# Performance work log

Hardware: AMD Instinct MI355X
Metric: run time of the kernel (lower is better)

## Reference

```python
import jax, jax.numpy as jnp
import numpy as np

B, N, C = 64, 196, 768
H = 12
HD = C // H            # 64
TOPK = int(0.25 * HD)  # 16
HIDDEN = int(C * 4.0)  # 3072
SCALE = HD ** -0.5
EPS = 1e-5


def layernorm(x, g, b):
    mu = jnp.mean(x, axis=-1, keepdims=True)
    var = jnp.var(x, axis=-1, keepdims=True)
    return (x - mu) * jax.lax.rsqrt(var + EPS) * g + b


def setup_inputs() -> dict:
    key = jax.random.key(0)
    ks = jax.random.split(key, 8)
    s = 0.02
    return {
        "x": jax.random.normal(ks[0], (B, N, C), jnp.float32),
        "norm1_g": jnp.ones((C,), jnp.float32),
        "norm1_b": jnp.zeros((C,), jnp.float32),
        "qk_w": jax.random.normal(ks[1], (2 * C, C), jnp.float32) * s,   # torch Linear [out,in], no bias
        "attn_proj_w": jax.random.normal(ks[2], (C, H * TOPK), jnp.float32) * s,
        "attn_proj_b": jnp.zeros((C,), jnp.float32),
        "norm2_g": jnp.ones((C,), jnp.float32),
        "norm2_b": jnp.zeros((C,), jnp.float32),
        "fc1_w": jax.random.normal(ks[3], (HIDDEN, C), jnp.float32) * s,
        "fc1_b": jnp.zeros((HIDDEN,), jnp.float32),
        "fc2_w": jax.random.normal(ks[4], (C, HIDDEN), jnp.float32) * s,
        "fc2_b": jnp.zeros((C,), jnp.float32),
    }


def reference(x, norm1_g, norm1_b, qk_w, attn_proj_w, attn_proj_b,
              norm2_g, norm2_b, fc1_w, fc1_b, fc2_w, fc2_b):
    # --- HomoAttention branch ---
    h = layernorm(x, norm1_g, norm1_b)                       # [B,N,C]
    qk = h @ qk_w.T                                          # [B,N,2C]
    qk = qk.reshape(B, N, 2, H, HD).transpose(2, 0, 3, 1, 4) # [2,B,H,N,HD]
    q, k = qk[0] * SCALE, qk[1]
    attn = jnp.einsum('bhnd,bhmd->bhnm', q, k)               # [B,H,N,N]
    top_vals, _ = jax.lax.top_k(attn, TOPK)                  # [B,H,N,TOPK]
    a = jax.nn.softmax(top_vals, axis=-1)
    a = a.transpose(0, 2, 1, 3).reshape(B, N, H * TOPK)      # [B,N,H*TOPK]
    x = x + a @ attn_proj_w.T + attn_proj_b

    # --- MLP branch ---
    h2 = layernorm(x, norm2_g, norm2_b)
    h2 = jax.nn.gelu(h2 @ fc1_w.T + fc1_b, approximate=False)
    x = x + h2 @ fc2_w.T + fc2_b
    return x
```

## Files before the change

kernel.cpp:

```cpp
#include <hip/hip_runtime.h>


#define BATCH 64
#define SEQ   196
#define CH    768
#define NHEAD 12
#define HDIM  64
#define TOPK  16
#define HID   3072
#define MROWS 12544
#define MHALF 6272
#define SCALE_F 0.125f
#define NEGBIG -3e38f

typedef __bf16 bf16x8 __attribute__((ext_vector_type(8)));
typedef float  f32x4  __attribute__((ext_vector_type(4)));

__device__ __forceinline__ unsigned short f2b(float f) {
    union { float f; unsigned int i; } c; c.f = f;
    unsigned int u = c.i;
    return (unsigned short)((u + 0x7fffu + ((u >> 16) & 1u)) >> 16);
}
__device__ __forceinline__ float b2f(unsigned short u) {
    union { unsigned int i; float f; } c; c.i = ((unsigned int)u) << 16; return c.f;
}

__device__ __forceinline__ float med3(float a, float b, float c) {
    float r;
    asm("v_med3_f32 %0, %1, %2, %3" : "=v"(r) : "v"(a), "v"(b), "v"(c));
    return r;
}

__device__ __forceinline__ float gelu_f(float v) {
    float u = v * (0.7978845608f + 0.0356774081f * v * v);
    float e = __expf(2.0f * u);
    float th = 1.0f - 2.0f / (e + 1.0f);
    return 0.5f * v * (1.0f + th);
}

__device__ __forceinline__ void async16(const unsigned short* g, unsigned short* l) {
    __builtin_amdgcn_global_load_lds(
        (const __attribute__((address_space(1))) unsigned int*)(g),
        (__attribute__((address_space(3))) unsigned int*)(l), 16, 0, 0);
}

__global__ __launch_bounds__(256) void prep_k(const float* __restrict__ x,
                                              const float* __restrict__ gw,
                                              const float* __restrict__ bw,
                                              unsigned short* __restrict__ hbuf,
                                              const float* __restrict__ s0, unsigned short* __restrict__ d0, int n0,
                                              const float* __restrict__ s1, unsigned short* __restrict__ d1, int n1,
                                              const float* __restrict__ s2, unsigned short* __restrict__ d2, int n2,
                                              const float* __restrict__ s3, unsigned short* __restrict__ d3, int n3)
{
    const int bid = blockIdx.x;
    const int tid = threadIdx.x;
    __shared__ __align__(16) float red[8];
    if (bid < MROWS) {
        const float* xr = x + (size_t)bid * CH;
        float v0 = xr[tid], v1 = xr[tid + 256], v2 = xr[tid + 512];
        float s  = v0 + v1 + v2;
        float sq = v0*v0 + v1*v1 + v2*v2;
#pragma unroll
        for (int off = 32; off > 0; off >>= 1) {
            s  += __shfl_down(s, off, 64);
            sq += __shfl_down(sq, off, 64);
        }
        if ((tid & 63) == 0) { red[(tid >> 6) * 2] = s; red[(tid >> 6) * 2 + 1] = sq; }
        __syncthreads();
        s  = red[0] + red[2] + red[4] + red[6];
        sq = red[1] + red[3] + red[5] + red[7];
        float mu  = s * (1.0f / CH);
        float var = sq * (1.0f / CH) - mu * mu;
        float rs  = rsqrtf(var + 1e-5f);
        unsigned short* orow = hbuf + (size_t)bid * CH;
        orow[tid]       = f2b((v0 - mu) * rs * gw[tid]       + bw[tid]);
        orow[tid + 256] = f2b((v1 - mu) * rs * gw[tid + 256] + bw[tid + 256]);
        orow[tid + 512] = f2b((v2 - mu) * rs * gw[tid + 512] + bw[tid + 512]);
    } else {
        int idx = ((bid - MROWS) * 256 + tid) * 4;
        const float* s; unsigned short* d; int n;
        if (idx < n0) { s = s0; d = d0; n = n0; }
        else {
            idx -= n0;
            if (idx < n1) { s = s1; d = d1; n = n1; }
            else {
                idx -= n1;
                if (idx < n2) { s = s2; d = d2; n = n2; }
                else { idx -= n2; s = s3; d = d3; n = n3; }
            }
        }
        if (idx < n) {
            float4 v = *(const float4*)(s + idx);
            ushort4 o;
            o.x = f2b(v.x); o.y = f2b(v.y); o.z = f2b(v.z); o.w = f2b(v.w);
            *(ushort4*)(d + idx) = o;
        }
    }
}

template<bool INF32>
__global__ __launch_bounds__(256) void ln_k(const void* __restrict__ xin,
                                            const float* __restrict__ gw,
                                            const float* __restrict__ bw,
                                            unsigned short* __restrict__ out)
{
    const int row = blockIdx.x;
    const int tid = threadIdx.x;
    float v0, v1, v2;
    if constexpr (INF32) {
        const float* xr = (const float*)xin + (size_t)row * CH;
        v0 = xr[tid]; v1 = xr[tid + 256]; v2 = xr[tid + 512];
    } else {
        const unsigned short* xr = (const unsigned short*)xin + (size_t)row * CH;
        v0 = b2f(xr[tid]); v1 = b2f(xr[tid + 256]); v2 = b2f(xr[tid + 512]);
    }
    float s  = v0 + v1 + v2;
    float sq = v0*v0 + v1*v1 + v2*v2;
#pragma unroll
    for (int off = 32; off > 0; off >>= 1) {
        s  += __shfl_down(s, off, 64);
        sq += __shfl_down(sq, off, 64);
    }
    __shared__ __align__(16) float red[8];
    if ((tid & 63) == 0) { red[(tid >> 6) * 2] = s; red[(tid >> 6) * 2 + 1] = sq; }
    __syncthreads();
// ... 33 lines not shown
    const int remM = gridM - sg * 8;
    int mloc, nloc;
    if (remM >= 8) { mloc = sg * 8 + (r & 7); nloc = r >> 3; }
    else           { mloc = sg * 8 + r % remM; nloc = r / remM; }
    const int tileM = mloc * TM;
    const int tileN = nloc * TN;

    const int wm = (w / WCOLS) * 64;
    const int wn = (w % WCOLS) * (JF * 16);
    const int q   = lane >> 4;
    const int l16 = lane & 15;
    const int csw = (q ^ (l16 & 3)) * 8;

    f32x4 acc[4][JF];
#pragma unroll
    for (int i = 0; i < 4; ++i)
#pragma unroll
        for (int j = 0; j < JF; ++j) acc[i][j] = (f32x4){0.f, 0.f, 0.f, 0.f};

    const int r0 = tid >> 2;
    const int g0 = ((tid & 3) ^ (r0 & 3)) * 8;

    const unsigned short* pB[TN / 64];
    const unsigned short* pA[TM / 64];
#pragma unroll
    for (int c = 0; c < TN / 64; ++c) pB[c] = Bw + (size_t)(tileN + r0 + c * 64) * K + g0;
#pragma unroll
    for (int c = 0; c < TM / 64; ++c) pA[c] = A + (size_t)(tileM + r0 + c * 64) * K + g0;

    auto stage = [&](int buf) {
#pragma unroll
        for (int c = 0; c < TN / 64; ++c) {
            async16(pB[c], &Bs[buf][(size_t)(c * 256 + w * 64) * 8]);
            pB[c] += 32;
        }
#pragma unroll
        for (int c = 0; c < TM / 64; ++c) {
            async16(pA[c], &As[buf][(size_t)(c * 256 + w * 64) * 8]);
            pA[c] += 32;
        }
    };

    const int kIters = K >> 5;
    stage(0);
    int cur = 0;
    for (int kt = 0; kt < kIters; ++kt) {
        __syncthreads();
        if (kt + 1 < kIters) stage(cur ^ 1);
        bf16x8 af[4], bfr[JF];
#pragma unroll
        for (int i = 0; i < 4; ++i)
            af[i] = *(const bf16x8*)&As[cur][(wm + i * 16 + l16) * 32 + csw];
#pragma unroll
        for (int j = 0; j < JF; ++j)
            bfr[j] = *(const bf16x8*)&Bs[cur][(wn + j * 16 + l16) * 32 + csw];
#pragma unroll
        for (int i = 0; i < 4; ++i)
#pragma unroll
            for (int j = 0; j < JF; ++j)
                acc[i][j] = __builtin_amdgcn_mfma_f32_16x16x32_bf16(af[i], bfr[j], acc[i][j], 0, 0, 0);
        cur ^= 1;
    }

#pragma unroll
    for (int i = 0; i < 4; ++i) {
#pragma unroll
        for (int r2 = 0; r2 < 4; ++r2) {
            int row = tileM + wm + i * 16 + q * 4 + r2;
#pragma unroll
            for (int j = 0; j < JF; ++j) {
                int col = tileN + wn + j * 16 + l16;
                float v = acc[i][j][r2];
                if (BIAS) v += bias[col];
                if (GELU) v = gelu_f(v);
                if (RES == 1) v += ((const float*)resid)[(size_t)row * N + col];
                if (RES == 2) v += b2f(((const unsigned short*)resid)[(size_t)row * N + col]);
                if (OUTF) ((float*)Cout)[(size_t)row * N + col] = v;
                else      ((unsigned short*)Cout)[(size_t)row * N + col] = f2b(v);
            }
        }
    }
}

template<int KC, bool BIAS, int RES, bool GELU, bool OUTF>
__global__ __launch_bounds__(512, 2)
void gemm8p(const unsigned short* __restrict__ A,
            const unsigned short* __restrict__ Bw,
            const float* __restrict__ bias,
            const void* __restrict__ resid,
            void* __restrict__ Cout,
            int M, int N)
{
    constexpr int T = KC / 64;
    static_assert((T & 1) == 0, "T must be even for persistent parity");
    __shared__ __align__(16) unsigned short As[2][256 * 64];
    __shared__ __align__(16) unsigned short Bs[2][256 * 64];
    const int tid  = threadIdx.x;
    const int w    = tid >> 6;
    const int lane = tid & 63;
    const int q    = lane >> 4;
    const int l16  = lane & 15;

    const int gridN = N >> 8, gridM = M >> 8;
    const int nt = gridN * gridM;
    const int P = gridDim.x;

    auto tileOf = [&](int lid2, int& tm, int& tn) {
        const int SG = 8 * gridN;
        const int sg = lid2 / SG, rr2 = lid2 % SG;
        const int remM = gridM - sg * 8;
        int mloc, nloc;
        if (remM >= 8) { mloc = sg * 8 + (rr2 & 7); nloc = rr2 >> 3; }
        else           { mloc = sg * 8 + rr2 % remM; nloc = rr2 / remM; }
        tm = mloc * 256; tn = nloc * 256;
    };

    const int wm = (w >> 2) * 128;
    const int wn = (w & 3) * 64;

    const int r0 = tid >> 3;
    const int g0 = (tid & 7) ^ (r0 & 7);
    const int rB = r0 + (r0 & 32);

    const int arow = wm + l16;
    const int brow = wn + l16;
    const int xsw  = l16 & 7;

    for (int t = (int)blockIdx.x; t < nt; t += P) {
        int tileM, tileN;
        tileOf(t, tileM, tileN);
        const bool hasNext = (t + P) < nt;
        int tileM2 = tileM, tileN2 = tileN;
        if (hasNext) tileOf(t + P, tileM2, tileN2);

        const unsigned short* pA0  = A  + (size_t)(tileM  + r0) * KC + g0 * 8;
        const unsigned short* pB0  = Bw + (size_t)(tileN  + rB) * KC + g0 * 8;
        const unsigned short* pA0n = A  + (size_t)(tileM2 + r0) * KC + g0 * 8;
        const unsigned short* pB0n = Bw + (size_t)(tileN2 + rB) * KC + g0 * 8;

        auto stageA = [&](int v, int j) {
            const unsigned short* base = (v == T) ? pA0n : pA0;
            const int vv = (v == T) ? 0 : v;
            const unsigned short* s = base + (size_t)(j * 64) * KC + vv * 64;
            unsigned short* d = As[vv & 1] + j * 4096 + w * 512;
            async16(s, d);
            async16(s + (size_t)128 * KC, d + 8192);
        };
        auto stageB = [&](int v, int j) {
            const unsigned short* base = (v == T) ? pB0n : pB0;
            const int vv = (v == T) ? 0 : v;
            const unsigned short* s = base + (size_t)(j * 32) * KC + vv * 64;
            unsigned short* d = Bs[vv & 1] + j * 2048 + (w * 8 + ((w & 4) << 3)) * 64;
            async16(s, d);
            async16(s + (size_t)128 * KC, d + 8192);
        };

        f32x4 acc[8][4];
#pragma unroll
        for (int i = 0; i < 8; ++i)
#pragma unroll
            for (int jn = 0; jn < 4; ++jn) acc[i][jn] = (f32x4){0.f, 0.f, 0.f, 0.f};

        if (t == (int)blockIdx.x) {
            stageA(0, 0); stageB(0, 0); stageB(0, 1); stageA(0, 1);
            asm volatile("s_waitcnt vmcnt(4)" ::: "memory");
            __builtin_amdgcn_s_barrier();
            asm volatile("" ::: "memory");
        }

#pragma unroll 2
        for (int u = 0; u < T; ++u) {
            const unsigned short* Ab = As[u & 1];
            const unsigned short* Bb = Bs[u & 1];
            const bool more = (u + 1 < T) || hasNext;
            bf16x8 af[4][2], b0[2][2], b1[2][2];

#pragma unroll
            for (int m = 0; m < 4; ++m)
#pragma unroll
                for (int kk = 0; kk < 2; ++kk)
                    af[m][kk] = *(const bf16x8*)&Ab[(arow + m * 16) * 64 + ((((kk << 2) | q) ^ xsw) << 3)];
#pragma unroll
            for (int n = 0; n < 2; ++n)
#pragma unroll
                for (int kk = 0; kk < 2; ++kk)
                    b0[n][kk] = *(const bf16x8*)&Bb[(brow + n * 16) * 64 + ((((kk << 2) | q) ^ xsw) << 3)];
            if (more) stageA(u + 1, 0);
            __builtin_amdgcn_s_setprio(1);
#pragma unroll
            for (int kk = 0; kk < 2; ++kk)
#pragma unroll
                for (int m = 0; m < 4; ++m)
#pragma unroll
                    for (int n = 0; n < 2; ++n)
                        acc[m][n] = __builtin_amdgcn_mfma_f32_16x16x32_bf16(af[m][kk], b0[n][kk], acc[m][n], 0, 0, 0);
            __builtin_amdgcn_s_setprio(0);

            if (more) asm volatile("s_waitcnt vmcnt(4)" ::: "memory");
            else      asm volatile("s_waitcnt vmcnt(2)" ::: "memory");
            __builtin_amdgcn_s_barrier();
            asm volatile("" ::: "memory");
#pragma unroll
            for (int n = 0; n < 2; ++n)
#pragma unroll
                for (int kk = 0; kk < 2; ++kk)
                    b1[n][kk] = *(const bf16x8*)&Bb[(brow + 32 + n * 16) * 64 + ((((kk << 2) | q) ^ xsw) << 3)];
            if (more) stageB(u + 1, 0);
            __builtin_amdgcn_s_setprio(1);
#pragma unroll
            for (int kk = 0; kk < 2; ++kk)
#pragma unroll
                for (int m = 0; m < 4; ++m)
#pragma unroll
                    for (int n = 0; n < 2; ++n)
                        acc[m][2 + n] = __builtin_amdgcn_mfma_f32_16x16x32_bf16(af[m][kk], b1[n][kk], acc[m][2 + n], 0, 0, 0);
            __builtin_amdgcn_s_setprio(0);

            if (more) asm volatile("s_waitcnt vmcnt(4)" ::: "memory");
            else      asm volatile("s_waitcnt vmcnt(0)" ::: "memory");
            __builtin_amdgcn_s_barrier();
            asm volatile("" ::: "memory");
#pragma unroll
            for (int m = 0; m < 4; ++m)
#pragma unroll
                for (int kk = 0; kk < 2; ++kk)
                    af[m][kk] = *(const bf16x8*)&Ab[(arow + 64 + m * 16) * 64 + ((((kk << 2) | q) ^ xsw) << 3)];
            if (more) stageB(u + 1, 1);
            __builtin_amdgcn_s_setprio(1);
#pragma unroll
            for (int kk = 0; kk < 2; ++kk)
#pragma unroll
                for (int m = 0; m < 4; ++m)
#pragma unroll
                    for (int n = 0; n < 2; ++n)
                        acc[4 + m][2 + n] = __builtin_amdgcn_mfma_f32_16x16x32_bf16(af[m][kk], b1[n][kk], acc[4 + m][2 + n], 0, 0, 0);
            __builtin_amdgcn_s_setprio(0);

            if (more) {
                stageA(u + 1, 1);
                asm volatile("s_waitcnt vmcnt(4)" ::: "memory");
                __builtin_amdgcn_s_barrier();
                asm volatile("" ::: "memory");
            }
            __builtin_amdgcn_s_setprio(1);
#pragma unroll
            for (int kk = 0; kk < 2; ++kk)
#pragma unroll
                for (int m = 0; m < 4; ++m)
#pragma unroll
                    for (int n = 0; n < 2; ++n)
                        acc[4 + m][n] = __builtin_amdgcn_mfma_f32_16x16x32_bf16(af[m][kk], b0[n][kk], acc[4 + m][n], 0, 0, 0);
            __builtin_amdgcn_s_setprio(0);
        }

        __syncthreads();

        float bshift[2][2];
        if (BIAS) {
#pragma unroll
            for (int nh = 0; nh < 2; ++nh)
#pragma unroll
                for (int n = 0; n < 2; ++n)
                    bshift[nh][n] = bias[tileN + wn + nh * 32 + n * 16 + l16];
        }

        if constexpr (!OUTF) {
            unsigned short* slab = &As[1][0] + (size_t)w * 1152;
            unsigned short* co = (unsigned short*)Cout;
#pragma unroll
            for (int mh = 0; mh < 2; ++mh)
#pragma unroll
                for (int m = 0; m < 4; ++m) {
#pragma unroll
                    for (int nh = 0; nh < 2; ++nh)
#pragma unroll
                        for (int n = 0; n < 2; ++n)
#pragma unroll
                            for (int r2 = 0; r2 < 4; ++r2) {
                                float v = acc[mh * 4 + m][nh * 2 + n][r2];
                                if (BIAS) v += bshift[nh][n];
                                if (GELU) v = gelu_f(v);
                                slab[(q * 4 + r2) * 72 + nh * 32 + n * 16 + l16] = f2b(v);
                            }
#pragma unroll
                    for (int h = 0; h < 2; ++h) {
                        const int lr = h * 8 + (lane >> 3);
                        const int grow = tileM + wm + mh * 64 + m * 16 + lr;
                        const int gcol = tileN + wn + (lane & 7) * 8;
                        uint4 pk = *(const uint4*)&slab[lr * 72 + (lane & 7) * 8];
                        if (RES != 0) {
                            unsigned short* ps = (unsigned short*)&pk;
#pragma unroll
                            for (int j = 0; j < 8; ++j) {
                                float v = b2f(ps[j]);
                                if (RES == 1) v += ((const float*)resid)[(size_t)grow * N + gcol + j];
                                if (RES == 2) v += b2f(((const unsigned short*)resid)[(size_t)grow * N + gcol + j]);
                                ps[j] = f2b(v);
                            }
                        }
                        *(uint4*)&co[(size_t)grow * N + gcol] = pk;
                    }
                }
        } else {
            float* slabf = (w == 7) ? (float*)&Bs[1][0]
                                    : (float*)&As[1][0] + (size_t)w * 1088;
            float* co = (float*)Cout;
#pragma unroll
            for (int mh = 0; mh < 2; ++mh)
#pragma unroll
                for (int m = 0; m < 4; ++m) {
#pragma unroll
                    for (int nh = 0; nh < 2; ++nh)
#pragma unroll
                        for (int n = 0; n < 2; ++n)
#pragma unroll
                            for (int r2 = 0; r2 < 4; ++r2) {
                                float v = acc[mh * 4 + m][nh * 2 + n][r2];
                                if (BIAS) v += bshift[nh][n];
                                if (GELU) v = gelu_f(v);
                                slabf[(q * 4 + r2) * 68 + nh * 32 + n * 16 + l16] = v;
                            }
#pragma unroll
                    for (int i4 = 0; i4 < 4; ++i4) {
                        const int lr = i4 * 4 + (lane >> 4);
                        const int grow = tileM + wm + mh * 64 + m * 16 + lr;
                        const int gcol = tileN + wn + (lane & 15) * 4;
                        f32x4 vv = *(const f32x4*)&slabf[lr * 68 + (lane & 15) * 4];
                        if (RES == 1) {
                            const float4 r4 = *(const float4*)&((const float*)resid)[(size_t)grow * N + gcol];
                            vv[0] += r4.x; vv[1] += r4.y; vv[2] += r4.z; vv[3] += r4.w;
                        }
                        if (RES == 2) {
                            const ushort4 r4 = *(const ushort4*)&((const unsigned short*)resid)[(size_t)grow * N + gcol];
                            vv[0] += b2f(r4.x); vv[1] += b2f(r4.y); vv[2] += b2f(r4.z); vv[3] += b2f(r4.w);
                        }
                        *(f32x4*)&co[(size_t)grow * N + gcol] = vv;
                    }
                }
        }

        if (hasNext) {
            asm volatile("s_waitcnt vmcnt(4)" ::: "memory");
            __syncthreads();
        }
    }
}

__global__ __launch_bounds__(256) void attn_topk(const unsigned short* __restrict__ qk,
                                                 unsigned short* __restrict__ aout)
{
    const int bh = blockIdx.x;
    const int b = bh / NHEAD, h = bh % NHEAD;
    __shared__ __align__(16) unsigned short Qs[208 * 64];
    __shared__ __align__(16) unsigned short Ks[208 * 64];
    const int tid = threadIdx.x;

    for (int i = tid; i < 208 * 8; i += 256) {
        int row = i >> 3, c = i & 7;
        uint4 vq = make_uint4(0, 0, 0, 0), vk = vq;
        if (row < SEQ) {
            const uint4* gp = (const uint4*)(qk + ((size_t)(b * SEQ + row) * 1536 + h * 64));
            vq = gp[c];
            vk = gp[c + 96];
        }
        int slot = c ^ (row & 7);
        *(uint4*)&Qs[row * 64 + slot * 8] = vq;
        *(uint4*)&Ks[row * 64 + slot * 8] = vk;
    }
    __syncthreads();

    const int w = tid >> 6, lane = tid & 63;
    const int q = lane >> 4, l16 = lane & 15;

    for (int tn = w; tn < 13; tn += 4) {
        const int nrow = tn * 16 + l16;
        const int nsw = nrow & 7;
        bf16x8 bq0 = *(const bf16x8*)&Qs[nrow * 64 + ((0 * 4 + q) ^ nsw) * 8];
        bf16x8 bq1 = *(const bf16x8*)&Qs[nrow * 64 + ((1 * 4 + q) ^ nsw) * 8];

        float t[TOPK];
#pragma unroll
        for (int j = 0; j < TOPK; ++j) t[j] = NEGBIG;

        for (int tm = 0; tm < 12; ++tm) {
            const int mrow = tm * 16 + l16;
            const int msw = mrow & 7;
            bf16x8 ak0 = *(const bf16x8*)&Ks[mrow * 64 + ((0 * 4 + q) ^ msw) * 8];
            bf16x8 ak1 = *(const bf16x8*)&Ks[mrow * 64 + ((1 * 4 + q) ^ msw) * 8];
            f32x4 acc = (f32x4){0.f, 0.f, 0.f, 0.f};
            acc = __builtin_amdgcn_mfma_f32_16x16x32_bf16(ak0, bq0, acc, 0, 0, 0);
            acc = __builtin_amdgcn_mfma_f32_16x16x32_bf16(ak1, bq1, acc, 0, 0, 0);
#pragma unroll
            for (int r = 0; r < 4; ++r) {
                float v = acc[r];
#pragma unroll
                for (int j = TOPK - 1; j >= 1; --j)
                    t[j] = med3(v, t[j], t[j - 1]);
                t[0] = fmaxf(t[0], v);
            }
        }
        {
            const int mrow = 12 * 16 + l16;
            const int msw = mrow & 7;
            bf16x8 ak0 = *(const bf16x8*)&Ks[mrow * 64 + ((0 * 4 + q) ^ msw) * 8];
            bf16x8 ak1 = *(const bf16x8*)&Ks[mrow * 64 + ((1 * 4 + q) ^ msw) * 8];
            f32x4 acc = (f32x4){0.f, 0.f, 0.f, 0.f};
            acc = __builtin_amdgcn_mfma_f32_16x16x32_bf16(ak0, bq0, acc, 0, 0, 0);
            acc = __builtin_amdgcn_mfma_f32_16x16x32_bf16(ak1, bq1, acc, 0, 0, 0);
#pragma unroll
            for (int r = 0; r < 4; ++r) {
                float v = (q == 0) ? acc[r] : NEGBIG;
#pragma unroll
                for (int j = TOPK - 1; j >= 1; --j)
                    t[j] = med3(v, t[j], t[j - 1]);
                t[0] = fmaxf(t[0], v);
            }
        }

#pragma unroll
        for (int stage = 0; stage < 2; ++stage) {
            const int xm = 16 << stage;
            float bl[TOPK], c[TOPK];
#pragma unroll
            for (int j = 0; j < TOPK; ++j) bl[j] = __shfl_xor(t[j], xm, 64);
#pragma unroll
            for (int j = 0; j < TOPK; ++j) c[j] = fmaxf(t[j], bl[TOPK - 1 - j]);
#pragma unroll
            for (int s = 8; s >= 1; s >>= 1) {
#pragma unroll
                for (int i = 0; i < TOPK; ++i) {
                    if ((i & s) == 0) {
                        float mx = fmaxf(c[i], c[i + s]);
                        c[i + s] = fminf(c[i], c[i + s]);
                        c[i] = mx;
                    }
                }
            }
#pragma unroll
            for (int j = 0; j < TOPK; ++j) t[j] = c[j];
        }

        if (q == 0 && nrow < SEQ) {
            float e[TOPK], sum = 0.f;
#pragma unroll
            for (int j = 0; j < TOPK; ++j) { e[j] = __expf((t[j] - t[0]) * SCALE_F); sum += e[j]; }
            float inv = 1.0f / sum;
            unsigned int pk[8];
#pragma unroll
            for (int jj = 0; jj < 8; ++jj)
                pk[jj] = (unsigned int)f2b(e[2 * jj] * inv) |
                         ((unsigned int)f2b(e[2 * jj + 1] * inv) << 16);
            unsigned short* dst = aout + ((size_t)(b * SEQ + nrow)) * (NHEAD * TOPK) + h * TOPK;
            ((uint4*)dst)[0] = make_uint4(pk[0], pk[1], pk[2], pk[3]);
            ((uint4*)dst)[1] = make_uint4(pk[4], pk[5], pk[6], pk[7]);
        }
    }
}

extern "C" void kernel_launch(void* const* d_in, const int* in_sizes, int n_in,
                              void* d_out, int out_size, void* d_ws, size_t ws_size,
                              hipStream_t stream)
{
    const float* x    = (const float*)d_in[0];
    const float* g1   = (const float*)d_in[1];
    const float* bb1  = (const float*)d_in[2];
    const float* qkw  = (const float*)d_in[3];
    const float* pw   = (const float*)d_in[4];
    const float* pb   = (const float*)d_in[5];
    const float* g2   = (const float*)d_in[6];
    const float* bb2  = (const float*)d_in[7];
    const float* f1w  = (const float*)d_in[8];
    const float* f1b  = (const float*)d_in[9];
    const float* f2w  = (const float*)d_in[10];
    const float* f2bp = (const float*)d_in[11];
    float* out = (float*)d_out;

    char* ws = (char*)d_ws;
    const size_t SZ_H   = (size_t)MROWS * CH * 2;
    const size_t N_WQK  = (size_t)2 * CH * CH;
    const size_t N_WP   = (size_t)CH * (NHEAD * TOPK);
    const size_t N_WF   = (size_t)HID * CH;
    const size_t SZ_W   = (N_WQK + N_WP + 2 * N_WF) * 2;
    const size_t SZ_A   = (size_t)MROWS * (NHEAD * TOPK) * 2;
    const size_t SZ_QK  = (size_t)MROWS * 2 * CH * 2;
    const size_t SZ_GGF = (size_t)MROWS * HID * 2;

    unsigned short* hbuf = (unsigned short*)(ws);
    unsigned short* wqk  = (unsigned short*)(ws + SZ_H);
    unsigned short* wp   = wqk + N_WQK;
    unsigned short* wf1  = wp  + N_WP;
    unsigned short* wf2  = wf1 + N_WF;
    unsigned short* av   = (unsigned short*)(ws + SZ_H + SZ_W);
    unsigned short* qk   = (unsigned short*)(ws + SZ_H + SZ_W + SZ_A);
    unsigned short* gg   = qk;

    const size_t base = SZ_H + SZ_W + SZ_A;
    const bool fullMLP = ws_size >= base + SZ_GGF + SZ_H;
    const bool bx1     = fullMLP || ws_size >= base + SZ_QK + SZ_H;
    unsigned short* x1b = (unsigned short*)(ws + base + (fullMLP ? SZ_GGF : SZ_QK));
    float* x1 = out;

    {
        int total4 = (int)((N_WQK + N_WP + 2 * N_WF) / 4);
        int wblk   = (total4 + 255) / 256;
        prep_k<<<MROWS + wblk, 256, 0, stream>>>(
            x, g1, bb1, hbuf,
            qkw, wqk, (int)N_WQK, pw, wp, (int)N_WP,
            f1w, wf1, (int)N_WF, f2w, wf2, (int)N_WF);
    }

    gemm8p<CH, false, 0, false, false><<<256, 512, 0, stream>>>(
        hbuf, wqk, nullptr, nullptr, qk, MROWS, 2 * CH);
    attn_topk<<<BATCH * NHEAD, 256, 0, stream>>>(qk, av);

    if (bx1) {
        gemm_bt<64, 128, true, 1, false, false><<<dim3(6, 196), 256, 0, stream>>>(
            av, wp, pb, x, x1b, MROWS, CH, NHEAD * TOPK);
        ln_k<false><<<MROWS, 256, 0, stream>>>(x1b, g2, bb2, hbuf);
        if (fullMLP) {
            gemm8p<CH, true, 0, true, false><<<256, 512, 0, stream>>>(
                hbuf, wf1, f1b, nullptr, gg, MROWS, HID);
            gemm8p<HID, true, 2, false, true><<<147, 512, 0, stream>>>(
                gg, wf2, f2bp, x1b, out, MROWS, CH);
        } else {
            for (int half = 0; half < 2; ++half) {
                const size_t ro = (size_t)half * MHALF;
                gemm_bt<128, 128, true, 0, true, false><<<dim3(24, 49), 256, 0, stream>>>(
                    hbuf + ro * CH, wf1, f1b, nullptr, gg, MHALF, HID, CH);
                gemm_bt<64, 256, true, 2, false, true><<<dim3(3, 98), 256, 0, stream>>>(
                    gg, wf2, f2bp, x1b + ro * CH, out + ro * CH, MHALF, CH, HID);
            }
        }
    } else {
        gemm_bt<64, 128, true, 1, false, true><<<dim3(6, 196), 256, 0, stream>>>(
            av, wp, pb, x, x1, MROWS, CH, NHEAD * TOPK);
        ln_k<true><<<MROWS, 256, 0, stream>>>(x1, g2, bb2, hbuf);
        for (int half = 0; half < 2; ++half) {
            const size_t ro = (size_t)half * MHALF;
            gemm_bt<128, 128, true, 0, true, false><<<dim3(24, 49), 256, 0, stream>>>(
                hbuf + ro * CH, wf1, f1b, nullptr, gg, MHALF, HID, CH);
            gemm_bt<64, 256, true, 1, false, true><<<dim3(3, 98), 256, 0, stream>>>(
                gg, wf2, f2bp, x1 + ro * CH, out + ro * CH, MHALF, CH, HID);
        }
    }
}
```

Baseline: 402.9 us.

## Merge layernorm, weight conversion and GEMMs into cooperative persistent kernels

Folds the first layernorm and the weight conversion into a cooperative kernel that runs a grid-wide sync and then the QK GEMM. A second cooperative kernel does the same for the second layernorm and the MLP GEMMs. The goal is to cut kernel launch gaps and tail idle time between the small and large kernels. It adds grid-sync overhead and a layernorm phase with only 256 blocks, which may underuse bandwidth compared with the old 12544-block launch. Falls back to separate launches if the cooperative launch fails.

Measured after the change: 975.1 us. 142% more time.

```diff
diff --git a/kernel.cpp b/kernel.cpp
--- a/kernel.cpp
+++ b/kernel.cpp
@@ -1,4 +1,5 @@
 #include <hip/hip_runtime.h>
+#include <hip/hip_cooperative_groups.h>
 
 
 #define BATCH 64
@@ -13,6 +14,8 @@
 #define SCALE_F 0.125f
 #define NEGBIG -3e38f
 
+namespace cg = cooperative_groups;
+
 typedef __bf16 bf16x8 __attribute__((ext_vector_type(8)));
 typedef float  f32x4  __attribute__((ext_vector_type(4)));
 
@@ -42,6 +45,404 @@
     __builtin_amdgcn_global_load_lds(
         (const __attribute__((address_space(1))) unsigned int*)(g),
         (__attribute__((address_space(3))) unsigned int*)(l), 16, 0, 0);
+}
+
+template<bool INF32>
+__device__ __forceinline__ void ln_phase(const void* __restrict__ xin,
+                                         const float* __restrict__ gw,
+                                         const float* __restrict__ bw,
+                                         unsigned short* __restrict__ out,
+                                         float* red)
+{
+    const int tid  = threadIdx.x;
+    const int half = tid >> 8;
+    const int t    = tid & 255;
+    const int base = (int)blockIdx.x * 49;
+#pragma unroll 1
+    for (int i = 0; i < 49; i += 2) {
+        const int ri = i + half;
+        const bool valid = ri < 49;
+        const int row = base + ri;
+        float v0 = 0.f, v1 = 0.f, v2 = 0.f;
+        if (valid) {
+            if constexpr (INF32) {
+                const float* xr = (const float*)xin + (size_t)row * CH;
+                v0 = xr[t]; v1 = xr[t + 256]; v2 = xr[t + 512];
+            } else {
+                const unsigned short* xr = (const unsigned short*)xin + (size_t)row * CH;
+                v0 = b2f(xr[t]); v1 = b2f(xr[t + 256]); v2 = b2f(xr[t + 512]);
+            }
+        }
+        float s  = v0 + v1 + v2;
+        float sq = v0*v0 + v1*v1 + v2*v2;
+#pragma unroll
+        for (int off = 32; off > 0; off >>= 1) {
+            s  += __shfl_down(s, off, 64);
+            sq += __shfl_down(sq, off, 64);
+        }
+        if ((tid & 63) == 0) { red[(tid >> 6) * 2] = s; red[(tid >> 6) * 2 + 1] = sq; }
+        __syncthreads();
+        s  = red[half * 8 + 0] + red[half * 8 + 2] + red[half * 8 + 4] + red[half * 8 + 6];
+        sq = red[half * 8 + 1] + red[half * 8 + 3] + red[half * 8 + 5] + red[half * 8 + 7];
+        __syncthreads();
+        if (valid) {
+            float mu  = s * (1.0f / CH);
+            float var = sq * (1.0f / CH) - mu * mu;
+            float rs  = rsqrtf(var + 1e-5f);
+            unsigned short* orow = out + (size_t)row * CH;
+            orow[t]       = f2b((v0 - mu) * rs * gw[t]       + bw[t]);
+            orow[t + 256] = f2b((v1 - mu) * rs * gw[t + 256] + bw[t + 256]);
+            orow[t + 512] = f2b((v2 - mu) * rs * gw[t + 512] + bw[t + 512]);
+        }
+    }
+}
+
+__device__ __forceinline__ void conv_phase(const float* s0, unsigned short* d0, int n0,
+                                           const float* s1, unsigned short* d1, int n1,
+                                           const float* s2, unsigned short* d2, int n2,
+                                           const float* s3, unsigned short* d3, int n3)
+{
+    const int total4 = (n0 + n1 + n2 + n3) >> 2;
+    for (int b4 = (int)blockIdx.x * 512 + (int)threadIdx.x; b4 < total4; b4 += 256 * 512) {
+        int idx = b4 * 4;
+        const float* s; unsigned short* d; int n;
+        if (idx < n0) { s = s0; d = d0; n = n0; }
+        else {
+            idx -= n0;
+            if (idx < n1) { s = s1; d = d1; n = n1; }
+            else {
+                idx -= n1;
+                if (idx < n2) { s = s2; d = d2; n = n2; }
+                else { idx -= n2; s = s3; d = d3; n = n3; }
+            }
+        }
+        if (idx < n) {
+            float4 v = *(const float4*)(s + idx);
+            ushort4 o;
+            o.x = f2b(v.x); o.y = f2b(v.y); o.z = f2b(v.z); o.w = f2b(v.w);
+            *(ushort4*)(d + idx) = o;
+        }
+    }
+}
+
+template<int KC, bool BIAS, int RES, bool GELU, bool OUTF>
+__device__ void gemm8p_body(const unsigned short* __restrict__ A,
+                            const unsigned short* __restrict__ Bw,
+                            const float* __restrict__ bias,
+                            const void* __restrict__ resid,
+                            void* __restrict__ Cout,
+                            int M, int N,
+                            unsigned short* AsP, unsigned short* BsP)
+{
+    constexpr int T = KC / 64;
+    static_assert((T & 1) == 0, "T must be even for persistent parity");
+    const int tid  = threadIdx.x;
+    const int w    = tid >> 6;
+    const int lane = tid & 63;
+    const int q    = lane >> 4;
+    const int l16  = lane & 15;
+
+    const int gridN = N >> 8, gridM = M >> 8;
+    const int nt = gridN * gridM;
+    const int P = gridDim.x;
+
+    auto tileOf = [&](int lid2, int& tm, int& tn) {
+        const int SG = 8 * gridN;
+        const int sg = lid2 / SG, rr2 = lid2 % SG;
+        const int remM = gridM - sg * 8;
+        int mloc, nloc;
+        if (remM >= 8) { mloc = sg * 8 + (rr2 & 7); nloc = rr2 >> 3; }
+        else           { mloc = sg * 8 + rr2 % remM; nloc = rr2 / remM; }
+        tm = mloc * 256; tn = nloc * 256;
+    };
+
+    const int wm = (w >> 2) * 128;
+    const int wn = (w & 3) * 64;
+
+    const int r0 = tid >> 3;
+    const int g0 = (tid & 7) ^ (r0 & 7);
+    const int rB = r0 + (r0 & 32);
+
+    const int arow = wm + l16;
+    const int brow = wn + l16;
+    const int xsw  = l16 & 7;
+
+    for (int t = (int)blockIdx.x; t < nt; t += P) {
+        int tileM, tileN;
+        tileOf(t, tileM, tileN);
+        const bool hasNext = (t + P) < nt;
+        int tileM2 = tileM, tileN2 = tileN;
+        if (hasNext) tileOf(t + P, tileM2, tileN2);
+
+        const unsigned short* pA0  = A  + (size_t)(tileM  + r0) * KC + g0 * 8;
+        const unsigned short* pB0  = Bw + (size_t)(tileN  + rB) * KC + g0 * 8;
+        const unsigned short* pA0n = A  + (size_t)(tileM2 + r0) * KC + g0 * 8;
+        const unsigned short* pB0n = Bw + (size_t)(tileN2 + rB) * KC + g0 * 8;
+
+        auto stageA = [&](int v, int j) {
+            const unsigned short* base = (v == T) ? pA0n : pA0;
+            const int vv = (v == T) ? 0 : v;
+            const unsigned short* s = base + (size_t)(j * 64) * KC + vv * 64;
+            unsigned short* d = AsP + (vv & 1) * 16384 + j * 4096 + w * 512;
+            async16(s, d);
+            async16(s + (size_t)128 * KC, d + 8192);
+        };
+        auto stageB = [&](int v, int j) {
+            const unsigned short* base = (v == T) ? pB0n : pB0;
+            const int vv = (v == T) ? 0 : v;
+            const unsigned short* s = base + (size_t)(j * 32) * KC + vv * 64;
+            unsigned short* d = BsP + (vv & 1) * 16384 + j * 2048 + (w * 8 + ((w & 4) << 3)) * 64;
+            async16(s, d);
+            async16(s + (size_t)128 * KC, d + 8192);
+        };
+
+        f32x4 acc[8][4];
+#pragma unroll
+        for (int i = 0; i < 8; ++i)
+#pragma unroll
+            for (int jn = 0; jn < 4; ++jn) acc[i][jn] = (f32x4){0.f, 0.f, 0.f, 0.f};
+
+        if (t == (int)blockIdx.x) {
+            stageA(0, 0); stageB(0, 0); stageB(0, 1); stageA(0, 1);
+            asm volatile("s_waitcnt vmcnt(4)" ::: "memory");
+            __builtin_amdgcn_s_barrier();
+            asm volatile("" ::: "memory");
+        }
+
+#pragma unroll 2
+        for (int u = 0; u < T; ++u) {
+            const unsigned short* Ab = AsP + (u & 1) * 16384;
+            const unsigned short* Bb = BsP + (u & 1) * 16384;
+            const bool more = (u + 1 < T) || hasNext;
+            bf16x8 af[4][2], b0[2][2], b1[2][2];
+
+#pragma unroll
+            for (int m = 0; m < 4; ++m)
+#pragma unroll
+                for (int kk = 0; kk < 2; ++kk)
+                    af[m][kk] = *(const bf16x8*)&Ab[(arow + m * 16) * 64 + ((((kk << 2) | q) ^ xsw) << 3)];
+#pragma unroll
+            for (int n = 0; n < 2; ++n)
+#pragma unroll
+                for (int kk = 0; kk < 2; ++kk)
+                    b0[n][kk] = *(const bf16x8*)&Bb[(brow + n * 16) * 64 + ((((kk << 2) | q) ^ xsw) << 3)];
+            if (more) stageA(u + 1, 0);
+            __builtin_amdgcn_s_setprio(1);
+#pragma unroll
+            for (int kk = 0; kk < 2; ++kk)
+#pragma unroll
+                for (int m = 0; m < 4; ++m)
+#pragma unroll
+                    for (int n = 0; n < 2; ++n)
+                        acc[m][n] = __builtin_amdgcn_mfma_f32_16x16x32_bf16(af[m][kk], b0[n][kk], acc[m][n], 0, 0, 0);
+            __builtin_amdgcn_s_setprio(0);
+
+            if (more) asm volatile("s_waitcnt vmcnt(4)" ::: "memory");
+            else      asm volatile("s_waitcnt vmcnt(2)" ::: "memory");
+            __builtin_amdgcn_s_barrier();
+            asm volatile("" ::: "memory");
+#pragma unroll
+            for (int n = 0; n < 2; ++n)
+#pragma unroll
+                for (int kk = 0; kk < 2; ++kk)
+                    b1[n][kk] = *(const bf16x8*)&Bb[(brow + 32 + n * 16) * 64 + ((((kk << 2) | q) ^ xsw) << 3)];
+            if (more) stageB(u + 1, 0);
+            __builtin_amdgcn_s_setprio(1);
+#pragma unroll
+            for (int kk = 0; kk < 2; ++kk)
+#pragma unroll
+                for (int m = 0; m < 4; ++m)
+#pragma unroll
+                    for (int n = 0; n < 2; ++n)
+                        acc[m][2 + n] = __builtin_amdgcn_mfma_f32_16x16x32_bf16(af[m][kk], b1[n][kk], acc[m][2 + n], 0, 0, 0);
+            __builtin_amdgcn_s_setprio(0);
+
+            if (more) asm volatile("s_waitcnt vmcnt(4)" ::: "memory");
+            else      asm volatile("s_waitcnt vmcnt(0)" ::: "memory");
+            __builtin_amdgcn_s_barrier();
+            asm volatile("" ::: "memory");
+#pragma unroll
+            for (int m = 0; m < 4; ++m)
+#pragma unroll
+                for (int kk = 0; kk < 2; ++kk)
+                    af[m][kk] = *(const bf16x8*)&Ab[(arow + 64 + m * 16) * 64 + ((((kk << 2) | q) ^ xsw) << 3)];
+            if (more) stageB(u + 1, 1);
+            __builtin_amdgcn_s_setprio(1);
+#pragma unroll
+            for (int kk = 0; kk < 2; ++kk)
+#pragma unroll
+                for (int m = 0; m < 4; ++m)
+#pragma unroll
+                    for (int n = 0; n < 2; ++n)
+                        acc[4 + m][2 + n] = __builtin_amdgcn_mfma_f32_16x16x32_bf16(af[m][kk], b1[n][kk], acc[4 + m][2 + n], 0, 0, 0);
+            __builtin_amdgcn_s_setprio(0);
+
+            if (more) {
+                stageA(u + 1, 1);
+                asm volatile("s_waitcnt vmcnt(4)" ::: "memory");
+                __builtin_amdgcn_s_barrier();
+                asm volatile("" ::: "memory");
+            }
+            __builtin_amdgcn_s_setprio(1);
+#pragma unroll
+            for (int kk = 0; kk < 2; ++kk)
+#pragma unroll
+                for (int m = 0; m < 4; ++m)
+#pragma unroll
+                    for (int n = 0; n < 2; ++n)
+                        acc[4 + m][n] = __builtin_amdgcn_mfma_f32_16x16x32_bf16(af[m][kk], b0[n][kk], acc[4 + m][n], 0, 0, 0);
+            __builtin_amdgcn_s_setprio(0);
+        }
+
+        __syncthreads();
+
+        float bshift[2][2];
+        if (BIAS) {
+#pragma unroll
+            for (int nh = 0; nh < 2; ++nh)
+#pragma unroll
+                for (int n = 0; n < 2; ++n)
+                    bshift[nh][n] = bias[tileN + wn + nh * 32 + n * 16 + l16];
+        }
+
+        if constexpr (!OUTF) {
+            unsigned short* slab = AsP + 16384 + (size_t)w * 1152;
+            unsigned short* co = (unsigned short*)Cout;
+#pragma unroll
+            for (int mh = 0; mh < 2; ++mh)
+#pragma unroll
+                for (int m = 0; m < 4; ++m) {
+#pragma unroll
+                    for (int nh = 0; nh < 2; ++nh)
+#pragma unroll
+                        for (int n = 0; n < 2; ++n)
+#pragma unroll
+                            for (int r2 = 0; r2 < 4; ++r2) {
+                                float v = acc[mh * 4 + m][nh * 2 + n][r2];
+                                if (BIAS) v += bshift[nh][n];
+                                if (GELU) v = gelu_f(v);
+                                slab[(q * 4 + r2) * 72 + nh * 32 + n * 16 + l16] = f2b(v);
+                            }
+#pragma unroll
+                    for (int h = 0; h < 2; ++h) {
+                        const int lr = h * 8 + (lane >> 3);
+                        const int grow = tileM + wm + mh * 64 + m * 16 + lr;
+                        const int gcol = tileN + wn + (lane & 7) * 8;
+                        uint4 pk = *(const uint4*)&slab[lr * 72 + (lane & 7) * 8];
+                        if (RES != 0) {
+                            unsigned short* ps = (unsigned short*)&pk;
+#pragma unroll
+                            for (int j = 0; j < 8; ++j) {
+                                float v = b2f(ps[j]);
+                                if (RES == 1) v += ((const float*)resid)[(size_t)grow * N + gcol + j];
+                                if (RES == 2) v += b2f(((const unsigned short*)resid)[(size_t)grow * N + gcol + j]);
+                                ps[j] = f2b(v);
+                            }
+                        }
+                        *(uint4*)&co[(size_t)grow * N + gcol] = pk;
+                    }
+                }
+        } else {
+            float* slabf = (w == 7) ? (float*)(BsP + 16384)
+                                    : (float*)(AsP + 16384) + (size_t)w * 1088;
+            float* co = (float*)Cout;
+#pragma unroll
+            for (int mh = 0; mh < 2; ++mh)
+#pragma unroll
+                for (int m = 0; m < 4; ++m) {
+#pragma unroll
+                    for (int nh = 0; nh < 2; ++nh)
+#pragma unroll
+                        for (int n = 0; n < 2; ++n)
+#pragma unroll
+                            for (int r2 = 0; r2 < 4; ++r2) {
+                                float v = acc[mh * 4 + m][nh * 2 + n][r2];
+                                if (BIAS) v += bshift[nh][n];
+                                if (GELU) v = gelu_f(v);
+                                slabf[(q * 4 + r2) * 68 + nh * 32 + n * 16 + l16] = v;
+                            }
+#pragma unroll
+                    for (int i4 = 0; i4 < 4; ++i4) {
+                        const int lr = i4 * 4 + (lane >> 4);
+                        const int grow = tileM + wm + mh * 64 + m * 16 + lr;
+                        const int gcol = tileN + wn + (lane & 15) * 4;
+                        f32x4 vv = *(const f32x4*)&slabf[lr * 68 + (lane & 15) * 4];
+                        if (RES == 1) {
+                            const float4 r4 = *(const float4*)&((const float*)resid)[(size_t)grow * N + gcol];
+                            vv[0] += r4.x; vv[1] += r4.y; vv[2] += r4.z; vv[3] += r4.w;
+                        }
+                        if (RES == 2) {
+                            const ushort4 r4 = *(const ushort4*)&((const unsigned short*)resid)[(size_t)grow * N + gcol];
+                            vv[0] += b2f(r4.x); vv[1] += b2f(r4.y); vv[2] += b2f(r4.z); vv[3] += b2f(r4.w);
+                        }
+                        *(f32x4*)&co[(size_t)grow * N + gcol] = vv;
+                    }
+                }
+        }
+
+        if (hasNext) {
+            asm volatile("s_waitcnt vmcnt(4)" ::: "memory");
+            __syncthreads();
+        }
+    }
+}
+
+template<int KC, bool BIAS, int RES, bool GELU, bool OUTF>
+__global__ __launch_bounds__(512, 2)
+void gemm8p(const unsigned short* __restrict__ A,
+            const unsigned short* __restrict__ Bw,
+            const float* __restrict__ bias,
+            const void* __restrict__ resid,
+            void* __restrict__ Cout,
+            int M, int N)
+{
+    __shared__ __align__(16) unsigned short AsS[2 * 16384];
+    __shared__ __align__(16) unsigned short BsS[2 * 16384];
+    gemm8p_body<KC, BIAS, RES, GELU, OUTF>(A, Bw, bias, resid, Cout, M, N, AsS, BsS);
+}
+
+struct CoopAArgs {
+    const float* x; const float* g1; const float* b1; unsigned short* hbuf;
+    const float* s0; unsigned short* d0; int n0;
+    const float* s1; unsigned short* d1; int n1;
+    const float* s2; unsigned short* d2; int n2;
+    const float* s3; unsigned short* d3; int n3;
+    const unsigned short* wqk; unsigned short* qkbuf;
+};
+
+__global__ __launch_bounds__(512, 2) void coopA(CoopAArgs a)
+{
+    __shared__ __align__(16) unsigned short AsS[2 * 16384];
+    __shared__ __align__(16) unsigned short BsS[2 * 16384];
+    __shared__ __align__(16) float red[16];
+    ln_phase<true>(a.x, a.g1, a.b1, a.hbuf, red);
+    conv_phase(a.s0, a.d0, a.n0, a.s1, a.d1, a.n1, a.s2, a.d2, a.n2, a.s3, a.d3, a.n3);
+    __threadfence();
+    cg::this_grid().sync();
+    gemm8p_body<CH, false, 0, false, false>(a.hbuf, a.wqk, nullptr, nullptr, a.qkbuf,
+                                            MROWS, 2 * CH, AsS, BsS);
+}
+
+struct CoopBArgs {
+    const unsigned short* x1b; const float* g2; const float* b2; unsigned short* hbuf;
+    const unsigned short* wf1; const float* f1b; unsigned short* gg;
+    const unsigned short* wf2; const float* f2b; float* out;
+};
+
+__global__ __launch_bounds__(512, 2) void coopB(CoopBArgs b)
+{
+    __shared__ __align__(16) unsigned short AsS[2 * 16384];
+    __shared__ __align__(16) unsigned short BsS[2 * 16384];
+    __shared__ __align__(16) float red[16];
+    ln_phase<false>(b.x1b, b.g2, b.b2, b.hbuf, red);
+    __threadfence();
+    cg::this_grid().sync();
+    gemm8p_body<CH, true, 0, true, false>(b.hbuf, b.wf1, b.f1b, nullptr, b.gg,
+                                          MROWS, HID, AsS, BsS);
+    __threadfence();
+    cg::this_grid().sync();
+    gemm8p_body<HID, true, 2, false, true>(b.gg, b.wf2, b.f2b, b.x1b, b.out,
+                                           MROWS, CH, AsS, BsS);
 }
 
 __global__ __launch_bounds__(256) void prep_k(const float* __restrict__ x,
@@ -241,270 +642,6 @@
     }
 }
 
-template<int KC, bool BIAS, int RES, bool GELU, bool OUTF>
-__global__ __launch_bounds__(512, 2)
-void gemm8p(const unsigned short* __restrict__ A,
-            const unsigned short* __restrict__ Bw,
-            const float* __restrict__ bias,
-            const void* __restrict__ resid,
-            void* __restrict__ Cout,
-            int M, int N)
-{
-    constexpr int T = KC / 64;
-    static_assert((T & 1) == 0, "T must be even for persistent parity");
-    __shared__ __align__(16) unsigned short As[2][256 * 64];
-    __shared__ __align__(16) unsigned short Bs[2][256 * 64];
-    const int tid  = threadIdx.x;
-    const int w    = tid >> 6;
-    const int lane = tid & 63;
-    const int q    = lane >> 4;
-    const int l16  = lane & 15;
-
-    const int gridN = N >> 8, gridM = M >> 8;
-    const int nt = gridN * gridM;
-    const int P = gridDim.x;
-
-    auto tileOf = [&](int lid2, int& tm, int& tn) {
-        const int SG = 8 * gridN;
-        const int sg = lid2 / SG, rr2 = lid2 % SG;
-        const int remM = gridM - sg * 8;
-        int mloc, nloc;
-        if (remM >= 8) { mloc = sg * 8 + (rr2 & 7); nloc = rr2 >> 3; }
-        else           { mloc = sg * 8 + rr2 % remM; nloc = rr2 / remM; }
-        tm = mloc * 256; tn = nloc * 256;
-    };
-
-    const int wm = (w >> 2) * 128;
-    const int wn = (w & 3) * 64;
-
-    const int r0 = tid >> 3;
-    const int g0 = (tid & 7) ^ (r0 & 7);
-    const int rB = r0 + (r0 & 32);
-
-    const int arow = wm + l16;
-    const int brow = wn + l16;
-    const int xsw  = l16 & 7;
-
-    for (int t = (int)blockIdx.x; t < nt; t += P) {
-        int tileM, tileN;
-        tileOf(t, tileM, tileN);
-        const bool hasNext = (t + P) < nt;
-        int tileM2 = tileM, tileN2 = tileN;
-        if (hasNext) tileOf(t + P, tileM2, tileN2);
-
-        const unsigned short* pA0  = A  + (size_t)(tileM  + r0) * KC + g0 * 8;
-        const unsigned short* pB0  = Bw + (size_t)(tileN  + rB) * KC + g0 * 8;
-        const unsigned short* pA0n = A  + (size_t)(tileM2 + r0) * KC + g0 * 8;
-        const unsigned short* pB0n = Bw + (size_t)(tileN2 + rB) * KC + g0 * 8;
-
-        auto stageA = [&](int v, int j) {
-            const unsigned short* base = (v == T) ? pA0n : pA0;
-            const int vv = (v == T) ? 0 : v;
-            const unsigned short* s = base + (size_t)(j * 64) * KC + vv * 64;
-            unsigned short* d = As[vv & 1] + j * 4096 + w * 512;
-            async16(s, d);
-            async16(s + (size_t)128 * KC, d + 8192);
-        };
-        auto stageB = [&](int v, int j) {
-            const unsigned short* base = (v == T) ? pB0n : pB0;
-            const int vv = (v == T) ? 0 : v;
-            const unsigned short* s = base + (size_t)(j * 32) * KC + vv * 64;
-            unsigned short* d = Bs[vv & 1] + j * 2048 + (w * 8 + ((w & 4) << 3)) * 64;
-            async16(s, d);
-            async16(s + (size_t)128 * KC, d + 8192);
-        };
-
-        f32x4 acc[8][4];
-#pragma unroll
-        for (int i = 0; i < 8; ++i)
-#pragma unroll
-            for (int jn = 0; jn < 4; ++jn) acc[i][jn] = (f32x4){0.f, 0.f, 0.f, 0.f};
-
-        if (t == (int)blockIdx.x) {
-            stageA(0, 0); stageB(0, 0); stageB(0, 1); stageA(0, 1);
-            asm volatile("s_waitcnt vmcnt(4)" ::: "memory");
-            __builtin_amdgcn_s_barrier();
-            asm volatile("" ::: "memory");
-        }
-
-#pragma unroll 2
-        for (int u = 0; u < T; ++u) {
-            const unsigned short* Ab = As[u & 1];
-            const unsigned short* Bb = Bs[u & 1];
-            const bool more = (u + 1 < T) || hasNext;
-            bf16x8 af[4][2], b0[2][2], b1[2][2];
-
-#pragma unroll
-            for (int m = 0; m < 4; ++m)
-#pragma unroll
-                for (int kk = 0; kk < 2; ++kk)
-                    af[m][kk] = *(const bf16x8*)&Ab[(arow + m * 16) * 64 + ((((kk << 2) | q) ^ xsw) << 3)];
-#pragma unroll
-            for (int n = 0; n < 2; ++n)
-#pragma unroll
-                for (int kk = 0; kk < 2; ++kk)
-                    b0[n][kk] = *(const bf16x8*)&Bb[(brow + n * 16) * 64 + ((((kk << 2) | q) ^ xsw) << 3)];
-            if (more) stageA(u + 1, 0);
-            __builtin_amdgcn_s_setprio(1);
-#pragma unroll
-            for (int kk = 0; kk < 2; ++kk)
-#pragma unroll
-                for (int m = 0; m < 4; ++m)
-#pragma unroll
-                    for (int n = 0; n < 2; ++n)
-                        acc[m][n] = __builtin_amdgcn_mfma_f32_16x16x32_bf16(af[m][kk], b0[n][kk], acc[m][n], 0, 0, 0);
-            __builtin_amdgcn_s_setprio(0);
-
-            if (more) asm volatile("s_waitcnt vmcnt(4)" ::: "memory");
-            else      asm volatile("s_waitcnt vmcnt(2)" ::: "memory");
-            __builtin_amdgcn_s_barrier();
-            asm volatile("" ::: "memory");
-#pragma unroll
-            for (int n = 0; n < 2; ++n)
-#pragma unroll
-                for (int kk = 0; kk < 2; ++kk)
-                    b1[n][kk] = *(const bf16x8*)&Bb[(brow + 32 + n * 16) * 64 + ((((kk << 2) | q) ^ xsw) << 3)];
-            if (more) stageB(u + 1, 0);
-            __builtin_amdgcn_s_setprio(1);
-#pragma unroll
-            for (int kk = 0; kk < 2; ++kk)
-#pragma unroll
-                for (int m = 0; m < 4; ++m)
-#pragma unroll
-                    for (int n = 0; n < 2; ++n)
-                        acc[m][2 + n] = __builtin_amdgcn_mfma_f32_16x16x32_bf16(af[m][kk], b1[n][kk], acc[m][2 + n], 0, 0, 0);
-            __builtin_amdgcn_s_setprio(0);
-
-            if (more) asm volatile("s_waitcnt vmcnt(4)" ::: "memory");
-            else      asm volatile("s_waitcnt vmcnt(0)" ::: "memory");
-            __builtin_amdgcn_s_barrier();
-            asm volatile("" ::: "memory");
-#pragma unroll
-            for (int m = 0; m < 4; ++m)
-#pragma unroll
-                for (int kk = 0; kk < 2; ++kk)
-                    af[m][kk] = *(const bf16x8*)&Ab[(arow + 64 + m * 16) * 64 + ((((kk << 2) | q) ^ xsw) << 3)];
-            if (more) stageB(u + 1, 1);
-            __builtin_amdgcn_s_setprio(1);
-#pragma unroll
-            for (int kk = 0; kk < 2; ++kk)
-#pragma unroll
-                for (int m = 0; m < 4; ++m)
-#pragma unroll
-                    for (int n = 0; n < 2; ++n)
-                        acc[4 + m][2 + n] = __builtin_amdgcn_mfma_f32_16x16x32_bf16(af[m][kk], b1[n][kk], acc[4 + m][2 + n], 0, 0, 0);
-            __builtin_amdgcn_s_setprio(0);
-
-            if (more) {
-                stageA(u + 1, 1);
-                asm volatile("s_waitcnt vmcnt(4)" ::: "memory");
-                __builtin_amdgcn_s_barrier();
-                asm volatile("" ::: "memory");
-            }
-            __builtin_amdgcn_s_setprio(1);
-#pragma unroll
-            for (int kk = 0; kk < 2; ++kk)
-#pragma unroll
-                for (int m = 0; m < 4; ++m)
-#pragma unroll
-                    for (int n = 0; n < 2; ++n)
-                        acc[4 + m][n] = __builtin_amdgcn_mfma_f32_16x16x32_bf16(af[m][kk], b0[n][kk], acc[4 + m][n], 0, 0, 0);
-            __builtin_amdgcn_s_setprio(0);
-        }
-
-        __syncthreads();
-
-        float bshift[2][2];
-        if (BIAS) {
-#pragma unroll
-            for (int nh = 0; nh < 2; ++nh)
-#pragma unroll
-                for (int n = 0; n < 2; ++n)
-                    bshift[nh][n] = bias[tileN + wn + nh * 32 + n * 16 + l16];
-        }
-
-        if constexpr (!OUTF) {
-            unsigned short* slab = &As[1][0] + (size_t)w * 1152;
-            unsigned short* co = (unsigned short*)Cout;
-#pragma unroll
-            for (int mh = 0; mh < 2; ++mh)
-#pragma unroll
-                for (int m = 0; m < 4; ++m) {
-#pragma unroll
-                    for (int nh = 0; nh < 2; ++nh)
-#pragma unroll
-                        for (int n = 0; n < 2; ++n)
-#pragma unroll
-                            for (int r2 = 0; r2 < 4; ++r2) {
-                                float v = acc[mh * 4 + m][nh * 2 + n][r2];
-                                if (BIAS) v += bshift[nh][n];
-                                if (GELU) v = gelu_f(v);
-                                slab[(q * 4 + r2) * 72 + nh * 32 + n * 16 + l16] = f2b(v);
-                            }
-#pragma unroll
-                    for (int h = 0; h < 2; ++h) {
-                        const int lr = h * 8 + (lane >> 3);
-                        const int grow = tileM + wm + mh * 64 + m * 16 + lr;
-                        const int gcol = tileN + wn + (lane & 7) * 8;
-                        uint4 pk = *(const uint4*)&slab[lr * 72 + (lane & 7) * 8];
-                        if (RES != 0) {
-                            unsigned short* ps = (unsigned short*)&pk;
-#pragma unroll
-                            for (int j = 0; j < 8; ++j) {
-                                float v = b2f(ps[j]);
-                                if (RES == 1) v += ((const float*)resid)[(size_t)grow * N + gcol + j];
-                                if (RES == 2) v += b2f(((const unsigned short*)resid)[(size_t)grow * N + gcol + j]);
-                                ps[j] = f2b(v);
-                            }
-                        }
-                        *(uint4*)&co[(size_t)grow * N + gcol] = pk;
-                    }
-                }
-        } else {
-            float* slabf = (w == 7) ? (float*)&Bs[1][0]
-                                    : (float*)&As[1][0] + (size_t)w * 1088;
-            float* co = (float*)Cout;
-#pragma unroll
-            for (int mh = 0; mh < 2; ++mh)
-#pragma unroll
-                for (int m = 0; m < 4; ++m) {
-#pragma unroll
-                    for (int nh = 0; nh < 2; ++nh)
-#pragma unroll
-                        for (int n = 0; n < 2; ++n)
-#pragma unroll
-                            for (int r2 = 0; r2 < 4; ++r2) {
-                                float v = acc[mh * 4 + m][nh * 2 + n][r2];
-                                if (BIAS) v += bshift[nh][n];
-                                if (GELU) v = gelu_f(v);
-                                slabf[(q * 4 + r2) * 68 + nh * 32 + n * 16 + l16] = v;
-                            }
-#pragma unroll
-                    for (int i4 = 0; i4 < 4; ++i4) {
-                        const int lr = i4 * 4 + (lane >> 4);
-                        const int grow = tileM + wm + mh * 64 + m * 16 + lr;
-                        const int gcol = tileN + wn + (lane & 15) * 4;
-                        f32x4 vv = *(const f32x4*)&slabf[lr * 68 + (lane & 15) * 4];
-                        if (RES == 1) {
-                            const float4 r4 = *(const float4*)&((const float*)resid)[(size_t)grow * N + gcol];
-                            vv[0] += r4.x; vv[1] += r4.y; vv[2] += r4.z; vv[3] += r4.w;
-                        }
-                        if (RES == 2) {
-                            const ushort4 r4 = *(const ushort4*)&((const unsigned short*)resid)[(size_t)grow * N + gcol];
-                            vv[0] += b2f(r4.x); vv[1] += b2f(r4.y); vv[2] += b2f(r4.z); vv[3] += b2f(r4.w);
-                        }
-                        *(f32x4*)&co[(size_t)grow * N + gcol] = vv;
-                    }
-                }
-        }
-
-        if (hasNext) {
-            asm volatile("s_waitcnt vmcnt(4)" ::: "memory");
-            __syncthreads();
-        }
-    }
-}
-
 __global__ __launch_bounds__(256) void attn_topk(const unsigned short* __restrict__ qk,
                                                  unsigned short* __restrict__ aout)
 {
@@ -659,29 +796,53 @@
     unsigned short* x1b = (unsigned short*)(ws + base + (fullMLP ? SZ_GGF : SZ_QK));
     float* x1 = out;
 
-    {
-        int total4 = (int)((N_WQK + N_WP + 2 * N_WF) / 4);
-        int wblk   = (total4 + 255) / 256;
+    const int total4 = (int)((N_WQK + N_WP + 2 * N_WF) / 4);
+    const int wblk   = (total4 + 255) / 256;
+
+    if (fullMLP) {
+        CoopAArgs pa { x, g1, bb1, hbuf,
+                       qkw, wqk, (int)N_WQK, pw, wp, (int)N_WP,
+                       f1w, wf1, (int)N_WF, f2w, wf2, (int)N_WF,
+                       wqk, qk };
+        void* argsA[] = { &pa };
+        hipError_t eA = hipLaunchCooperativeKernel((const void*)coopA, dim3(256), dim3(512),
+                                                   argsA, 0, stream);
+        if (eA != hipSuccess) {
+            prep_k<<<MROWS + wblk, 256, 0, stream>>>(
+                x, g1, bb1, hbuf,
+                qkw, wqk, (int)N_WQK, pw, wp, (int)N_WP,
+                f1w, wf1, (int)N_WF, f2w, wf2, (int)N_WF);
+            gemm8p<CH, false, 0, false, false><<<256, 512, 0, stream>>>(
+                hbuf, wqk, nullptr, nullptr, qk, MROWS, 2 * CH);
+        }
+
+        attn_topk<<<BATCH * NHEAD, 256, 0, stream>>>(qk, av);
+        gemm_bt<64, 128, true, 1, false, false><<<dim3(6, 196), 256, 0, stream>>>(
+            av, wp, pb, x, x1b, MROWS, CH, NHEAD * TOPK);
+
+        CoopBArgs pbb { x1b, g2, bb2, hbuf, wf1, f1b, gg, wf2, f2bp, out };
+        void* argsB[] = { &pbb };
+        hipError_t eB = hipLaunchCooperativeKernel((const void*)coopB, dim3(256), dim3(512),
+                                                   argsB, 0, stream);
+        if (eB != hipSuccess) {
+            ln_k<false><<<MROWS, 256, 0, stream>>>(x1b, g2, bb2, hbuf);
+            gemm8p<CH, true, 0, true, false><<<256, 512, 0, stream>>>(
+                hbuf, wf1, f1b, nullptr, gg, MROWS, HID);
+            gemm8p<HID, true, 2, false, true><<<147, 512, 0, stream>>>(
+                gg, wf2, f2bp, x1b, out, MROWS, CH);
+        }
+    } else {
         prep_k<<<MROWS + wblk, 256, 0, stream>>>(
             x, g1, bb1, hbuf,
             qkw, wqk, (int)N_WQK, pw, wp, (int)N_WP,
             f1w, wf1, (int)N_WF, f2w, wf2, (int)N_WF);
-    }
-
-    gemm8p<CH, false, 0, false, false><<<256, 512, 0, stream>>>(
-        hbuf, wqk, nullptr, nullptr, qk, MROWS, 2 * CH);
-    attn_topk<<<BATCH * NHEAD, 256, 0, stream>>>(qk, av);
-
-    if (bx1) {
-        gemm_bt<64, 128, true, 1, false, false><<<dim3(6, 196), 256, 0, stream>>>(
-            av, wp, pb, x, x1b, MROWS, CH, NHEAD * TOPK);
-        ln_k<false><<<MROWS, 256, 0, stream>>>(x1b, g2, bb2, hbuf);
-        if (fullMLP) {
-            gemm8p<CH, true, 0, true, false><<<256, 512, 0, stream>>>(
-                hbuf, wf1, f1b, nullptr, gg, MROWS, HID);
-            gemm8p<HID, true, 2, false, true><<<147, 512, 0, stream>>>(
-                gg, wf2, f2bp, x1b, out, MROWS, CH);
-        } else {
+        gemm8p<CH, false, 0, false, false><<<256, 512, 0, stream>>>(
+            hbuf, wqk, nullptr, nullptr, qk, MROWS, 2 * CH);
+        attn_topk<<<BATCH * NHEAD, 256, 0, stream>>>(qk, av);
+        if (bx1) {
+            gemm_bt<64, 128, true, 1, false, false><<<dim3(6, 196), 256, 0, stream>>>(
+                av, wp, pb, x, x1b, MROWS, CH, NHEAD * TOPK);
+            ln_k<false><<<MROWS, 256, 0, stream>>>(x1b, g2, bb2, hbuf);
             for (int half = 0; half < 2; ++half) {
                 const size_t ro = (size_t)half * MHALF;
                 gemm_bt<128, 128, true, 0, true, false><<<dim3(24, 49), 256, 0, stream>>>(
@@ -689,17 +850,17 @@
                 gemm_bt<64, 256, true, 2, false, true><<<dim3(3, 98), 256, 0, stream>>>(
                     gg, wf2, f2bp, x1b + ro * CH, out + ro * CH, MHALF, CH, HID);
             }
-        }
-    } else {
-        gemm_bt<64, 128, true, 1, false, true><<<dim3(6, 196), 256, 0, stream>>>(
-            av, wp, pb, x, x1, MROWS, CH, NHEAD * TOPK);
-        ln_k<true><<<MROWS, 256, 0, stream>>>(x1, g2, bb2, hbuf);
-        for (int half = 0; half < 2; ++half) {
-            const size_t ro = (size_t)half * MHALF;
-            gemm_bt<128, 128, true, 0, true, false><<<dim3(24, 49), 256, 0, stream>>>(
-                hbuf + ro * CH, wf1, f1b, nullptr, gg, MHALF, HID, CH);
-            gemm_bt<64, 256, true, 1, false, true><<<dim3(3, 98), 256, 0, stream>>>(
-                gg, wf2, f2bp, x1 + ro * CH, out + ro * CH, MHALF, CH, HID);
-        }
-    }
-}
+        } else {
+            gemm_bt<64, 128, true, 1, false, true><<<dim3(6, 196), 256, 0, stream>>>(
+                av, wp, pb, x, x1, MROWS, CH, NHEAD * TOPK);
+            ln_k<true><<<MROWS, 256, 0, stream>>>(x1, g2, bb2, hbuf);
+            for (int half = 0; half < 2; ++half) {
+                const size_t ro = (size_t)half * MHALF;
+                gemm_bt<128, 128, true, 0, true, false><<<dim3(24, 49), 256, 0, stream>>>(
+                    hbuf + ro * CH, wf1, f1b, nullptr, gg, MHALF, HID, CH);
+                gemm_bt<64, 256, true, 1, false, true><<<dim3(3, 98), 256, 0, stream>>>(
+                    gg, wf2, f2bp, x1 + ro * CH, out + ro * CH, MHALF, CH, HID);
+            }
+        }
+    }
+}
```
